# Kernel tuning notes

Measured on AMD Instinct MI355X. Metric: run time of the kernel, lower is better.

Reference implementation:

```python
import jax, jax.numpy as jnp
import numpy as np

N = 4096
STD = 0.01


def setup_inputs() -> dict:
    key = jax.random.key(0)
    ks = jax.random.split(key, 16)
    p = lambda k, shape: STD * jax.random.normal(k, shape, dtype=jnp.float32)
    return {
        "t": 0,
        "x": jax.random.normal(ks[0], (N, 1), dtype=jnp.float32),
        "A": jax.random.normal(ks[1], (N, N), dtype=jnp.float32),
        # MLP_A: 2 -> 16 -> 16 -> 1 (ReLU between hidden layers), torch (out,in) layout
        "WA0": p(ks[2], (16, 2)), "bA0": p(ks[3], (16,)),
        "WA1": p(ks[4], (16, 16)), "bA1": p(ks[5], (16,)),
        "WA2": p(ks[6], (1, 16)), "bA2": p(ks[7], (1,)),
        # MLP: 1 -> 16 -> 1 (ReLU after first layer)
        "Wm0": p(ks[8], (16, 1)), "bm0": p(ks[9], (16,)),
        "Wm1": p(ks[10], (1, 16)), "bm1": p(ks[11], (1,)),
        # linear_A: 2 -> 1, no bias; linear_f: 1 -> 1, no bias
        "wA": p(ks[12], (1, 2)),
        "wf": p(ks[13], (1, 1)),
    }


def reference(t, x, A, WA0, bA0, WA1, bA1, WA2, bA2, Wm0, bm0, Wm1, bm1, wA, wf):
    n = x.shape[0]
    # node MLP branch: hidden_list[0] == 1 != 0
    x_N = jax.nn.relu(x @ Wm0.T + bm0) @ Wm1.T + bm1 + x @ wf.T  # (n, 1)
    # all-pairs features: x_a[i, j] = (x_i, x_j)
    x1 = jnp.broadcast_to(x, (n, n))       # row i = x_i repeated
    x2 = jnp.broadcast_to(x.T, (n, n))     # row i = full x vector
    x_a = jnp.stack((x1, x2), axis=-1)     # (n, n, 2)
    # edge MLP (2 -> 16 -> 16 -> 1) + skip linear_A (2 -> 1)
    h = jax.nn.relu(x_a @ WA0.T + bA0)     # (n, n, 16)
    h = jax.nn.relu(h @ WA1.T + bA1)       # (n, n, 16)
    x_e = (h @ WA2.T + bA2)[..., 0]        # (n, n)
    x_12 = (x_a @ wA.T)[..., 0]            # (n, n)
    # adjacency-weighted reduction over neighbors (dim=1)
    x_A = jnp.sum(A * (x_e + x_12), axis=1, keepdims=True)  # (n, 1)
    return x_N + x_A
```

## Files before the change

### kernel.cpp

```cpp
#include <hip/hip_runtime.h>
#include <hip/hip_bf16.h>


#define NN 4096

typedef __fp16 half8  __attribute__((ext_vector_type(8)));
typedef __fp16 half2v __attribute__((ext_vector_type(2)));
typedef __attribute__((ext_vector_type(4)))  float f32x4;
typedef __attribute__((ext_vector_type(16))) float f32x16;

__device__ __forceinline__ half2v cvt2(float lo, float hi) {
    return __builtin_amdgcn_cvt_pkrtz(lo, hi);
}

__global__ __launch_bounds__(256, 6) void odef_kernel(
    const float* __restrict__ x,  const float* __restrict__ A,
    const float* __restrict__ WA0, const float* __restrict__ bA0,
    const float* __restrict__ WA1, const float* __restrict__ bA1,
    const float* __restrict__ WA2, const float* __restrict__ bA2,
    const float* __restrict__ Wm0, const float* __restrict__ bm0,
    const float* __restrict__ Wm1, const float* __restrict__ bm1,
    const float* __restrict__ wA,  const float* __restrict__ wf,
    float* __restrict__ out)
{
    __shared__ float xs[NN];
    __shared__ float partial[4];

    const int tid  = threadIdx.x;
    const int wave = tid >> 6;
    const int lane = tid & 63;
    const int n    = lane & 31;
    const int half = lane >> 5;
    const int row  = blockIdx.x * 2 + (wave >> 1);
    const int jbase = (wave & 1) * (NN / 2);

    {
        const f32x4* xsrc = (const f32x4*)x;
        f32x4* xdst = (f32x4*)xs;
        #pragma unroll
        for (int i = 0; i < 4; ++i)
            xdst[tid + 256 * i] = xsrc[tid + 256 * i];
    }

    const float xi = x[row];

    union { half2v h2[4]; half8 h8; } au;
    #pragma unroll
    for (int p = 0; p < 4; ++p) {
        float lo = 0.f, hi = 0.f;
        if (n < 16) {
            int k = half * 8 + p * 2;
            lo = WA1[n * 16 + k];
            hi = WA1[n * 16 + k + 1];
        }
        au.h2[p] = cvt2(lo, hi);
    }

    half2v u2h[4], w2h[4];
    #pragma unroll
    for (int p = 0; p < 4; ++p) {
        int k0 = half * 8 + p * 2;
        u2h[p] = cvt2(fmaf(WA0[2 * k0],     xi, bA0[k0]),
                      fmaf(WA0[2 * k0 + 2], xi, bA0[k0 + 1]));
        w2h[p] = cvt2(WA0[2 * k0 + 1], WA0[2 * k0 + 3]);
    }

    half2v wa2h[4], bb[4];
    #pragma unroll
    for (int p = 0; p < 4; ++p) {
        int r  = 2 * p;
        int m0 = (r & 3) + 8 * (r >> 2) + 4 * half;
        wa2h[p] = cvt2(WA2[m0], WA2[m0 + 1]);
        bb[p]   = cvt2(bA1[m0], bA1[m0 + 1]);
    }

    const float wA1h = half ? 0.f : wA[1];
    const float c0h  = half ? 0.f : (bA2[0] + wA[0] * xi);
    const half2v z2 = { (__fp16)0.f, (__fp16)0.f };
    const f32x16 zc = {};

    const f32x4* __restrict__ ab  = (const f32x4*)(A + (size_t)row * NN + jbase);
    const f32x4* __restrict__ xls = (const f32x4*)(xs + jbase);

    float acc0 = 0.f, acc1 = 0.f;

    auto body = [&](const f32x4 xv, const f32x4 av) {
        #pragma unroll
        for (int q = 0; q < 4; q += 2) {
            half2v xg0 = cvt2(xv[q], xv[q]);
            union { half2v h2[4]; half8 h8; } b0;
            #pragma unroll
            for (int p = 0; p < 4; ++p)
                b0.h2[p] = __builtin_elementwise_max(w2h[p] * xg0 + u2h[p], z2);
            f32x16 d0 = __builtin_amdgcn_mfma_f32_32x32x16_f16(au.h8, b0.h8, zc, 0, 0, 0);

            half2v xg1 = cvt2(xv[q + 1], xv[q + 1]);
            union { half2v h2[4]; half8 h8; } b1;
            #pragma unroll
            for (int p = 0; p < 4; ++p)
                b1.h2[p] = __builtin_elementwise_max(w2h[p] * xg1 + u2h[p], z2);
            f32x16 d1 = __builtin_amdgcn_mfma_f32_32x32x16_f16(au.h8, b1.h8, zc, 0, 0, 0);

            {
                float pp = fmaf(wA1h, xv[q], c0h);
                #pragma unroll
                for (int p = 0; p < 4; ++p) {
                    half2v t = __builtin_elementwise_max(
                        cvt2(d0[2 * p], d0[2 * p + 1]) + bb[p], z2);
                    pp = __builtin_amdgcn_fdot2(t, wa2h[p], pp, false);
                }
                acc0 = fmaf(av[q], pp, acc0);
            }
            {
                float pp = fmaf(wA1h, xv[q + 1], c0h);
                #pragma unroll
                for (int p = 0; p < 4; ++p) {
                    half2v t = __builtin_elementwise_max(
                        cvt2(d1[2 * p], d1[2 * p + 1]) + bb[p], z2);
                    pp = __builtin_amdgcn_fdot2(t, wa2h[p], pp, false);
                }
                acc1 = fmaf(av[q + 1], pp, acc1);
            }
        }
    };

    __syncthreads();

    int o = n;
    f32x4 a0 = ab[o];
    f32x4 a1 = ab[o + 32];
    f32x4 a2 = ab[o + 64];
    f32x4 xv = xls[o];
    for (int it = 0; it < 16; ++it) {
        const int opref = o + ((it + 3 < 16) ? 96 : 0);
        const int oxn   = o + ((it + 1 < 16) ? 32 : 0);
        f32x4 a3 = ab[opref];
        f32x4 xn = xls[oxn];
        body(xv, a0);
        a0 = a1; a1 = a2; a2 = a3; xv = xn;
        o += 32;
    }

    float acc = acc0 + acc1;
    #pragma unroll
    for (int off = 32; off > 0; off >>= 1)
        acc += __shfl_xor(acc, off);
    if (lane == 0) partial[wave] = acc;
    __syncthreads();

    if (lane == 0 && (wave & 1) == 0) {
        float xn = fmaf(wf[0], xi, bm1[0]);
        #pragma unroll
        for (int h = 0; h < 16; ++h)
            xn = fmaf(Wm1[h], fmaxf(fmaf(Wm0[h], xi, bm0[h]), 0.f), xn);
        out[row] = xn + partial[wave] + partial[wave + 1];
    }
}

extern "C" void kernel_launch(void* const* d_in, const int* in_sizes, int n_in,
                              void* d_out, int out_size, void* d_ws, size_t ws_size,
                              hipStream_t stream) {
    const float* x   = (const float*)d_in[1];
    const float* A   = (const float*)d_in[2];
    const float* WA0 = (const float*)d_in[3];
    const float* bA0 = (const float*)d_in[4];
    const float* WA1 = (const float*)d_in[5];
    const float* bA1 = (const float*)d_in[6];
    const float* WA2 = (const float*)d_in[7];
    const float* bA2 = (const float*)d_in[8];
    const float* Wm0 = (const float*)d_in[9];
    const float* bm0 = (const float*)d_in[10];
    const float* Wm1 = (const float*)d_in[11];
    const float* bm1 = (const float*)d_in[12];
    const float* wA  = (const float*)d_in[13];
    const float* wf  = (const float*)d_in[14];
    float* out = (float*)d_out;

    odef_kernel<<<NN / 2, 256, 0, stream>>>(x, A, WA0, bA0, WA1, bA1, WA2, bA2,
                                            Wm0, bm0, Wm1, bm1, wA, wf, out);
}
```

Measured before the change: 143.8 us.

## Stream A rows into LDS ring via async global_load_lds, one row per wave

Each wave now owns a full row of A instead of half a row, which removes the cross-wave shared-memory reduction and the second barrier. A rows are streamed through a 4-deep per-wave LDS ring using global_load_lds with explicit vmcnt waits, replacing the register-based prefetch. Occupancy hint drops from 6 to 4 blocks per SM and the grid halves. LDS use grows by 16 KB per block, which may limit occupancy. The hand-written waitcnt scheduling also depends on the compiler not issuing other vector-memory loads in the loop.

```diff
diff --git a/kernel.cpp b/kernel.cpp
--- a/kernel.cpp
+++ b/kernel.cpp
@@ -13,7 +13,7 @@
     return __builtin_amdgcn_cvt_pkrtz(lo, hi);
 }
 
-__global__ __launch_bounds__(256, 6) void odef_kernel(
+__global__ __launch_bounds__(256, 4) void odef_kernel(
     const float* __restrict__ x,  const float* __restrict__ A,
     const float* __restrict__ WA0, const float* __restrict__ bA0,
     const float* __restrict__ WA1, const float* __restrict__ bA1,
@@ -24,15 +24,14 @@
     float* __restrict__ out)
 {
     __shared__ float xs[NN];
-    __shared__ float partial[4];
+    __shared__ float ring[4][4][256];
 
     const int tid  = threadIdx.x;
     const int wave = tid >> 6;
     const int lane = tid & 63;
     const int n    = lane & 31;
     const int half = lane >> 5;
-    const int row  = blockIdx.x * 2 + (wave >> 1);
-    const int jbase = (wave & 1) * (NN / 2);
+    const int row  = blockIdx.x * 4 + wave;
 
     {
         const f32x4* xsrc = (const f32x4*)x;
@@ -43,6 +42,17 @@
     }
 
     const float xi = x[row];
+    const float* arow = A + (size_t)row * NN;
+
+    auto issue = [&](int pair) {
+        const float* src = arow + pair * 256 + lane * 4;
+        __builtin_amdgcn_global_load_lds(
+            (const __attribute__((address_space(1))) void*)src,
+            (__attribute__((address_space(3))) void*)&ring[wave][pair & 3][0],
+            16, 0, 0);
+    };
+
+    issue(0); issue(1); issue(2);
 
     union { half2v h2[4]; half8 h8; } au;
     #pragma unroll
@@ -78,9 +88,6 @@
     const float c0h  = half ? 0.f : (bA2[0] + wA[0] * xi);
     const half2v z2 = { (__fp16)0.f, (__fp16)0.f };
     const f32x16 zc = {};
-
-    const f32x4* __restrict__ ab  = (const f32x4*)(A + (size_t)row * NN + jbase);
-    const f32x4* __restrict__ xls = (const f32x4*)(xs + jbase);
 
     float acc0 = 0.f, acc1 = 0.f;
 
@@ -126,34 +133,42 @@
 
     __syncthreads();
 
-    int o = n;
-    f32x4 a0 = ab[o];
-    f32x4 a1 = ab[o + 32];
-    f32x4 a2 = ab[o + 64];
-    f32x4 xv = xls[o];
-    for (int it = 0; it < 16; ++it) {
-        const int opref = o + ((it + 3 < 16) ? 96 : 0);
-        const int oxn   = o + ((it + 1 < 16) ? 32 : 0);
-        f32x4 a3 = ab[opref];
-        f32x4 xn = xls[oxn];
-        body(xv, a0);
-        a0 = a1; a1 = a2; a2 = a3; xv = xn;
-        o += 32;
+    const f32x4* xls = (const f32x4*)xs;
+    f32x4 xv = xls[n];
+
+#define STEP(P, WN, DO_ISSUE)                                                \
+    {                                                                        \
+        if (DO_ISSUE) issue((P) + 3);                                        \
+        asm volatile("s_waitcnt vmcnt(" #WN ")" ::: "memory");               \
+        __builtin_amdgcn_sched_barrier(0);                                   \
+        const f32x4* sp = (const f32x4*)&ring[wave][(P) & 3][0];             \
+        f32x4 av0 = sp[n];                                                   \
+        f32x4 av1 = sp[32 + n];                                              \
+        f32x4 xn0 = xls[(2 * (P) + 1) * 32 + n];                             \
+        f32x4 xn1 = ((P) < 15) ? xls[(2 * (P) + 2) * 32 + n] : xn0;          \
+        body(xv, av0);                                                       \
+        body(xn0, av1);                                                      \
+        xv = xn1;                                                            \
     }
+
+    for (int P = 0; P < 13; ++P)
+        STEP(P, 3, true);
+    STEP(13, 2, false);
+    STEP(14, 1, false);
+    STEP(15, 0, false);
+#undef STEP
 
     float acc = acc0 + acc1;
     #pragma unroll
     for (int off = 32; off > 0; off >>= 1)
         acc += __shfl_xor(acc, off);
-    if (lane == 0) partial[wave] = acc;
-    __syncthreads();
 
-    if (lane == 0 && (wave & 1) == 0) {
+    if (lane == 0) {
         float xn = fmaf(wf[0], xi, bm1[0]);
         #pragma unroll
         for (int h = 0; h < 16; ++h)
             xn = fmaf(Wm1[h], fmaxf(fmaf(Wm0[h], xi, bm0[h]), 0.f), xn);
-        out[row] = xn + partial[wave] + partial[wave + 1];
+        out[row] = xn + acc;
     }
 }
 
@@ -176,6 +191,6 @@
     const float* wf  = (const float*)d_in[14];
     float* out = (float*)d_out;
 
-    odef_kernel<<<NN / 2, 256, 0, stream>>>(x, A, WA0, bA0, WA1, bA1, WA2, bA2,
+    odef_kernel<<<NN / 4, 256, 0, stream>>>(x, A, WA0, bA0, WA1, bA1, WA2, bA2,
                                             Wm0, bm0, Wm1, bm1, wA, wf, out);
 }
```

After: 142.7 us. No clear change (-0.8%).

## Stream A rows through an LDS ring via async global_load_lds, four rows per block

Applied to the files above, without the earlier changes.

Each block now handles four rows, with each wave covering a 1024-column slice of every row. Tiles of A are streamed into a 5-slot per-wave LDS ring using global_load_lds, with explicit vmcnt waits, replacing the register prefetch chain. The hidden bias bA1 is folded into the MFMA accumulator init, which removes a packed add per output pair. The cost is a larger LDS footprint (about 36 KB), lower launch-bounds occupancy (4 instead of 6), more live registers for the per-row biases, and half as many blocks.

```diff
diff --git a/kernel.cpp b/kernel.cpp
--- a/kernel.cpp
+++ b/kernel.cpp
@@ -13,7 +13,7 @@
     return __builtin_amdgcn_cvt_pkrtz(lo, hi);
 }
 
-__global__ __launch_bounds__(256, 6) void odef_kernel(
+__global__ __launch_bounds__(256, 4) void odef_kernel(
     const float* __restrict__ x,  const float* __restrict__ A,
     const float* __restrict__ WA0, const float* __restrict__ bA0,
     const float* __restrict__ WA1, const float* __restrict__ bA1,
@@ -24,15 +24,15 @@
     float* __restrict__ out)
 {
     __shared__ float xs[NN];
-    __shared__ float partial[4];
+    __shared__ float ring[4][5][256];
+    __shared__ float partial[4][4];
 
     const int tid  = threadIdx.x;
     const int wave = tid >> 6;
     const int lane = tid & 63;
     const int n    = lane & 31;
     const int half = lane >> 5;
-    const int row  = blockIdx.x * 2 + (wave >> 1);
-    const int jbase = (wave & 1) * (NN / 2);
+    const int r0   = blockIdx.x * 4;
 
     {
         const f32x4* xsrc = (const f32x4*)x;
@@ -41,8 +41,19 @@
         for (int i = 0; i < 4; ++i)
             xdst[tid + 256 * i] = xsrc[tid + 256 * i];
     }
-
-    const float xi = x[row];
+    const float xq0 = x[r0], xq1 = x[r0 + 1], xq2 = x[r0 + 2], xq3 = x[r0 + 3];
+
+    __syncthreads();
+
+    const float* abase = A + (size_t)r0 * NN + wave * 1024 + lane * 4;
+    auto issue = [&](int g, int slot) {
+        const float* src = abase + (g >> 2) * NN + (g & 3) * 256;
+        __builtin_amdgcn_global_load_lds(
+            (const __attribute__((address_space(1))) void*)src,
+            (__attribute__((address_space(3))) void*)&ring[wave][slot][0],
+            16, 0, 0);
+    };
+    issue(0, 0); issue(1, 1); issue(2, 2); issue(3, 3);
 
     union { half2v h2[4]; half8 h8; } au;
     #pragma unroll
@@ -56,33 +67,44 @@
         au.h2[p] = cvt2(lo, hi);
     }
 
-    half2v u2h[4], w2h[4];
+    half2v w2h[4], uA[4], uB[4], uC[4], uD[4];
     #pragma unroll
     for (int p = 0; p < 4; ++p) {
         int k0 = half * 8 + p * 2;
-        u2h[p] = cvt2(fmaf(WA0[2 * k0],     xi, bA0[k0]),
-                      fmaf(WA0[2 * k0 + 2], xi, bA0[k0 + 1]));
+        float alo = WA0[2 * k0],     ahi = WA0[2 * k0 + 2];
+        float blo = bA0[k0],         bhi = bA0[k0 + 1];
         w2h[p] = cvt2(WA0[2 * k0 + 1], WA0[2 * k0 + 3]);
-    }
-
-    half2v wa2h[4], bb[4];
+        uA[p] = cvt2(fmaf(alo, xq0, blo), fmaf(ahi, xq0, bhi));
+        uB[p] = cvt2(fmaf(alo, xq1, blo), fmaf(ahi, xq1, bhi));
+        uC[p] = cvt2(fmaf(alo, xq2, blo), fmaf(ahi, xq2, bhi));
+        uD[p] = cvt2(fmaf(alo, xq3, blo), fmaf(ahi, xq3, bhi));
+    }
+
+    half2v wa2h[4];
+    f32x16 cbias;
+    #pragma unroll
+    for (int r = 0; r < 16; ++r) cbias[r] = 0.f;
+    #pragma unroll
+    for (int r = 0; r < 8; ++r) {
+        int m = (r & 3) + 8 * (r >> 2) + 4 * half;
+        cbias[r] = bA1[m];
+    }
     #pragma unroll
     for (int p = 0; p < 4; ++p) {
-        int r  = 2 * p;
-        int m0 = (r & 3) + 8 * (r >> 2) + 4 * half;
+        int m0 = (2 * p & 3) + 8 * (2 * p >> 2) + 4 * half;
         wa2h[p] = cvt2(WA2[m0], WA2[m0 + 1]);
-        bb[p]   = cvt2(bA1[m0], bA1[m0 + 1]);
     }
 
     const float wA1h = half ? 0.f : wA[1];
-    const float c0h  = half ? 0.f : (bA2[0] + wA[0] * xi);
+    const float c0A = half ? 0.f : (bA2[0] + wA[0] * xq0);
+    const float c0B = half ? 0.f : (bA2[0] + wA[0] * xq1);
+    const float c0C = half ? 0.f : (bA2[0] + wA[0] * xq2);
+    const float c0D = half ? 0.f : (bA2[0] + wA[0] * xq3);
     const half2v z2 = { (__fp16)0.f, (__fp16)0.f };
-    const f32x16 zc = {};
-
-    const f32x4* __restrict__ ab  = (const f32x4*)(A + (size_t)row * NN + jbase);
-    const f32x4* __restrict__ xls = (const f32x4*)(xs + jbase);
 
     float acc0 = 0.f, acc1 = 0.f;
+    half2v u2h[4];
+    float c0h = 0.f;
 
     auto body = [&](const f32x4 xv, const f32x4 av) {
         #pragma unroll
@@ -92,21 +114,20 @@
             #pragma unroll
             for (int p = 0; p < 4; ++p)
                 b0.h2[p] = __builtin_elementwise_max(w2h[p] * xg0 + u2h[p], z2);
-            f32x16 d0 = __builtin_amdgcn_mfma_f32_32x32x16_f16(au.h8, b0.h8, zc, 0, 0, 0);
+            f32x16 d0 = __builtin_amdgcn_mfma_f32_32x32x16_f16(au.h8, b0.h8, cbias, 0, 0, 0);
 
             half2v xg1 = cvt2(xv[q + 1], xv[q + 1]);
             union { half2v h2[4]; half8 h8; } b1;
             #pragma unroll
             for (int p = 0; p < 4; ++p)
                 b1.h2[p] = __builtin_elementwise_max(w2h[p] * xg1 + u2h[p], z2);
-            f32x16 d1 = __builtin_amdgcn_mfma_f32_32x32x16_f16(au.h8, b1.h8, zc, 0, 0, 0);
+            f32x16 d1 = __builtin_amdgcn_mfma_f32_32x32x16_f16(au.h8, b1.h8, cbias, 0, 0, 0);
 
             {
                 float pp = fmaf(wA1h, xv[q], c0h);
                 #pragma unroll
                 for (int p = 0; p < 4; ++p) {
-                    half2v t = __builtin_elementwise_max(
-                        cvt2(d0[2 * p], d0[2 * p + 1]) + bb[p], z2);
+                    half2v t = __builtin_elementwise_max(cvt2(d0[2 * p], d0[2 * p + 1]), z2);
                     pp = __builtin_amdgcn_fdot2(t, wa2h[p], pp, false);
                 }
                 acc0 = fmaf(av[q], pp, acc0);
@@ -115,8 +136,7 @@
                 float pp = fmaf(wA1h, xv[q + 1], c0h);
                 #pragma unroll
                 for (int p = 0; p < 4; ++p) {
-                    half2v t = __builtin_elementwise_max(
-                        cvt2(d1[2 * p], d1[2 * p + 1]) + bb[p], z2);
+                    half2v t = __builtin_elementwise_max(cvt2(d1[2 * p], d1[2 * p + 1]), z2);
                     pp = __builtin_amdgcn_fdot2(t, wa2h[p], pp, false);
                 }
                 acc1 = fmaf(av[q + 1], pp, acc1);
@@ -124,36 +144,57 @@
         }
     };
 
+    int sl_c = 0;
+    int sl_i = 4;
+
+    auto consume = [&](int g) {
+        const int p4 = g & 3;
+        if (p4 == 0) {
+            const int rr = g >> 2;
+            #pragma unroll
+            for (int p = 0; p < 4; ++p)
+                u2h[p] = rr == 0 ? uA[p] : rr == 1 ? uB[p] : rr == 2 ? uC[p] : uD[p];
+            c0h = rr == 0 ? c0A : rr == 1 ? c0B : rr == 2 ? c0C : c0D;
+        }
+        const f32x4* sp = (const f32x4*)&ring[wave][sl_c][0];
+        sl_c = (sl_c == 4) ? 0 : sl_c + 1;
+        const f32x4* xq = (const f32x4*)(xs + wave * 1024 + p4 * 256);
+        f32x4 av0 = sp[n],      xv0 = xq[n];
+        f32x4 av1 = sp[32 + n], xv1 = xq[32 + n];
+        body(xv0, av0);
+        body(xv1, av1);
+        if (p4 == 3) {
+            float a = acc0 + acc1;
+            #pragma unroll
+            for (int off = 32; off > 0; off >>= 1)
+                a += __shfl_xor(a, off);
+            if (lane == 0) partial[g >> 2][wave] = a;
+            acc0 = 0.f; acc1 = 0.f;
+        }
+    };
+
+    for (int g = 0; g < 12; ++g) {
+        issue(g + 4, sl_i);
+        sl_i = (sl_i == 4) ? 0 : sl_i + 1;
+        asm volatile("s_waitcnt vmcnt(4)" ::: "memory");
+        __builtin_amdgcn_sched_barrier(0);
+        consume(g);
+    }
+    asm volatile("s_waitcnt vmcnt(0)" ::: "memory");
+    __builtin_amdgcn_sched_barrier(0);
+    for (int g = 12; g < 16; ++g)
+        consume(g);
+
     __syncthreads();
 
-    int o = n;
-    f32x4 a0 = ab[o];
-    f32x4 a1 = ab[o + 32];
-    f32x4 a2 = ab[o + 64];
-    f32x4 xv = xls[o];
-    for (int it = 0; it < 16; ++it) {
-        const int opref = o + ((it + 3 < 16) ? 96 : 0);
-        const int oxn   = o + ((it + 1 < 16) ? 32 : 0);
-        f32x4 a3 = ab[opref];
-        f32x4 xn = xls[oxn];
-        body(xv, a0);
-        a0 = a1; a1 = a2; a2 = a3; xv = xn;
-        o += 32;
-    }
-
-    float acc = acc0 + acc1;
-    #pragma unroll
-    for (int off = 32; off > 0; off >>= 1)
-        acc += __shfl_xor(acc, off);
-    if (lane == 0) partial[wave] = acc;
-    __syncthreads();
-
-    if (lane == 0 && (wave & 1) == 0) {
+    if (tid < 4) {
+        const float xi = x[r0 + tid];
+        float s = partial[tid][0] + partial[tid][1] + partial[tid][2] + partial[tid][3];
         float xn = fmaf(wf[0], xi, bm1[0]);
         #pragma unroll
         for (int h = 0; h < 16; ++h)
             xn = fmaf(Wm1[h], fmaxf(fmaf(Wm0[h], xi, bm0[h]), 0.f), xn);
-        out[row] = xn + partial[wave] + partial[wave + 1];
+        out[r0 + tid] = xn + s;
     }
 }
 
@@ -176,6 +217,6 @@
     const float* wf  = (const float*)d_in[14];
     float* out = (float*)d_out;
 
-    odef_kernel<<<NN / 2, 256, 0, stream>>>(x, A, WA0, bA0, WA1, bA1, WA2, bA2,
+    odef_kernel<<<NN / 4, 256, 0, stream>>>(x, A, WA0, bA0, WA1, bA1, WA2, bA2,
                                             Wm0, bm0, Wm1, bm1, wA, wf, out);
 }
```

Measured after the change: 146.0 us. About the same (+1.6%).
